# Performance work log

Measured on AMD Instinct MI355X. Metric: run time of the kernel, lower is better.

## Reference

```python
import jax, jax.numpy as jnp
import numpy as np


def _gru_cell(x, h, W_ih, W_hh, b_ih, b_hh):
    # torch.nn.GRUCell math; gate order (r, z, n). x: [.,D] or [1,D] (broadcast), h: [E,D]
    gi = x @ W_ih.T + b_ih            # [., 3D]
    gh = h @ W_hh.T + b_hh            # [E, 3D]
    i_r, i_z, i_n = jnp.split(gi, 3, axis=-1)
    h_r, h_z, h_n = jnp.split(gh, 3, axis=-1)
    r = jax.nn.sigmoid(i_r + h_r)
    z = jax.nn.sigmoid(i_z + h_z)
    n = jnp.tanh(i_n + r * h_n)
    return (1.0 - z) * n + z * h


def setup_inputs() -> dict:
    D = 256          # num_embed_units
    E = 200000       # neighbor edges of the seed
    N = E + 1        # nodes in the sampled subgraph (seed is node E)
    V = 500000       # entity vocab
    R = 1000         # relation vocab
    key = jax.random.key(0)
    ks = jax.random.split(key, 14)
    s = 1.0 / np.sqrt(D)  # torch default init bound
    inp = {
        "encoder_output": jax.random.normal(ks[0], (1, D), jnp.float32),
        "sample_mask": jax.random.normal(ks[1], (1, D), jnp.float32),
        "entity_table": jax.random.normal(ks[2], (V, D), jnp.float32) * 0.02,
        "rel_table": jax.random.normal(ks[3], (R, D), jnp.float32) * 0.02,
        "W_ih": jax.random.uniform(ks[4], (3 * D, D), jnp.float32, -s, s),
        "W_hh": jax.random.uniform(ks[5], (3 * D, D), jnp.float32, -s, s),
        "b_ih": jax.random.uniform(ks[6], (3 * D,), jnp.float32, -s, s),
        "b_hh": jax.random.uniform(ks[7], (3 * D,), jnp.float32, -s, s),
        "sub_W": jax.random.uniform(ks[8], (D, D), jnp.float32, -s, s),
        "sub_b": jax.random.uniform(ks[9], (D,), jnp.float32, -s, s),
        "obj_W": jax.random.uniform(ks[10], (D, D), jnp.float32, -s, s),
        "obj_b": jax.random.uniform(ks[11], (D,), jnp.float32, -s, s),
        "rel_ids": jax.random.randint(ks[12], (E,), 0, R, jnp.int64 if jax.config.jax_enable_x64 else jnp.int32),
        "tail_ids": jnp.arange(E, dtype=jnp.int32),
        "tails_state": jax.random.randint(ks[13], (E,), 0, 2, jnp.int32),
        "origin_ids": jax.random.randint(jax.random.fold_in(key, 99), (E,), 0, V, jnp.int32),
        "seed": E,
        "num_nodes": N,
    }
    return inp


def reference(encoder_output, sample_mask, entity_table, rel_table, W_ih, W_hh, b_ih, b_hh,
              sub_W, sub_b, obj_W, obj_b, rel_ids, tail_ids, tails_state, origin_ids, seed, num_nodes):
    D = encoder_output.shape[-1]
    # seed_state == 0 branch: sub = tanh(Linear(sample_mask))
    sub = jnp.tanh(sample_mask @ sub_W.T + sub_b)                      # [1, D]
    r0 = _gru_cell(encoder_output, sub, W_ih, W_hh, b_ih, b_hh)        # [1, D]
    # vectorized per-edge GRUCell: input r0 (broadcast), hidden = relation embedding
    rel_emb = rel_table[rel_ids]                                       # [E, D]
    rj = _gru_cell(r0, rel_emb, W_ih, W_hh, b_ih, b_hh)                # [E, D]
    obj = jnp.tanh(rj @ obj_W.T + obj_b)                               # [E, D]
    # tails with state==1 get their pretrained entity embedding instead
    from_table = entity_table[origin_ids]                              # [E, D]
    tail_vals = jnp.where((tails_state == 1)[:, None], from_table, obj)
    ent = jnp.zeros((num_nodes, D), dtype=encoder_output.dtype)
    ent = ent.at[seed].set(sub[0])
    ent = ent.at[tail_ids].set(tail_vals)
    return ent
```

## Files before the change

### kernel.cpp

```cpp
#include <hip/hip_runtime.h>
#include <hip/hip_bf16.h>

typedef unsigned short u16;
using bf16x8 = __attribute__((ext_vector_type(8))) short;
using f32x4  = __attribute__((ext_vector_type(4))) float;
using f4     = __attribute__((ext_vector_type(4))) float;

__device__ __forceinline__ u16 f2b(float f) {
    unsigned u = __float_as_uint(f);
    return (u16)((u + 0x7fffu + ((u >> 16) & 1u)) >> 16);
}
__device__ __forceinline__ float sigm(float x) { return 1.f / (1.f + expf(-x)); }

__device__ __forceinline__ bf16x8 pack8(const float* p) {
    float4 a = *(const float4*)p, b = *(const float4*)(p + 4);
    bf16x8 r;
    r[0] = (short)f2b(a.x); r[1] = (short)f2b(a.y);
    r[2] = (short)f2b(a.z); r[3] = (short)f2b(a.w);
    r[4] = (short)f2b(b.x); r[5] = (short)f2b(b.y);
    r[6] = (short)f2b(b.z); r[7] = (short)f2b(b.w);
    return r;
}

__device__ __forceinline__ float dot64(const float* __restrict__ w, const float* s) {
    float acc = 0.f;
    #pragma unroll
    for (int i = 0; i < 16; ++i) {
        float4 v = ((const float4*)w)[i];
        acc += v.x * s[i*4] + v.y * s[i*4+1] + v.z * s[i*4+2] + v.w * s[i*4+3];
    }
    return acc;
}

__global__ __launch_bounds__(256)
void k1a_sub_gi0(const float* __restrict__ enc, const float* __restrict__ mask,
                 const float* __restrict__ W_ih, const float* __restrict__ b_ih,
                 const float* __restrict__ sub_W, const float* __restrict__ sub_b,
                 float* __restrict__ sub_ws, float* __restrict__ gi0,
                 float* __restrict__ out, const int* __restrict__ seed_p)
{
    __shared__ float x_s[256];
    __shared__ float pA[256];
    const int b = blockIdx.x;
    const bool is_sub = (b < 4);
    const int tid = threadIdx.x;
    x_s[tid] = is_sub ? mask[tid] : enc[tid];
    __syncthreads();
    const int t = tid >> 2, g = tid & 3;
    if (is_sub) {
        const int i = b * 64 + t;
        pA[tid] = dot64(sub_W + (size_t)i * 256 + g * 64, x_s + g * 64);
    } else {
        const int j = (b - 4) * 64 + t;
        pA[tid] = dot64(W_ih + (size_t)j * 256 + g * 64, x_s + g * 64);
    }
    __syncthreads();
    if (tid < 64) {
        float v = pA[4*tid] + pA[4*tid+1] + pA[4*tid+2] + pA[4*tid+3];
        if (is_sub) {
            const int i = b * 64 + tid;
            float s = tanhf(v + sub_b[i]);
            sub_ws[i] = s;
            out[(size_t)seed_p[0] * 256 + i] = s;
        } else {
            const int j = (b - 4) * 64 + tid;
            gi0[j] = v + b_ih[j];
        }
    }
}

__global__ __launch_bounds__(256)
void k1b_gh0(const float* __restrict__ sub_ws, const float* __restrict__ W_hh,
             const float* __restrict__ b_hh, float* __restrict__ gh0)
{
    __shared__ float x_s[256];
    __shared__ float pA[256];
    const int tid = threadIdx.x;
    x_s[tid] = sub_ws[tid];
    __syncthreads();
    const int t = tid >> 2, g = tid & 3;
    const int j = blockIdx.x * 64 + t;
    pA[tid] = dot64(W_hh + (size_t)j * 256 + g * 64, x_s + g * 64);
    __syncthreads();
    if (tid < 64) {
        const int jj = blockIdx.x * 64 + tid;
        gh0[jj] = pA[4*tid] + pA[4*tid+1] + pA[4*tid+2] + pA[4*tid+3] + b_hh[jj];
    }
}

__global__ __launch_bounds__(256)
void k1c_gi1(const float* __restrict__ sub_ws, const float* __restrict__ gi0,
             const float* __restrict__ gh0, const float* __restrict__ W_ih,
             const float* __restrict__ b_ih, float* __restrict__ gi1)
{
    __shared__ float r0_s[256];
    __shared__ float pA[256];
    const int tid = threadIdx.x;
    {
        float rr = sigm(gi0[tid]       + gh0[tid]);
        float zz = sigm(gi0[256 + tid] + gh0[256 + tid]);
        float nn = tanhf(gi0[512 + tid] + rr * gh0[512 + tid]);
        r0_s[tid] = (1.f - zz) * nn + zz * sub_ws[tid];
    }
    __syncthreads();
    const int t = tid >> 2, g = tid & 3;
    const int j = blockIdx.x * 64 + t;
    pA[tid] = dot64(W_ih + (size_t)j * 256 + g * 64, r0_s + g * 64);
    __syncthreads();
    if (tid < 64) {
        const int jj = blockIdx.x * 64 + tid;
        gi1[jj] = pA[4*tid] + pA[4*tid+1] + pA[4*tid+2] + pA[4*tid+3] + b_ih[jj];
    }
}

__global__ __launch_bounds__(64)
void k2_ghcomb(const float* __restrict__ rel_table, const float* __restrict__ W_hh,
               const float* __restrict__ b_hh, const float* __restrict__ gi1,
               u16* __restrict__ rj, int R)
{
    const int l = threadIdx.x, m = l & 15, q = l >> 4;
    const int tt = blockIdx.y, jt = blockIdx.x;
    int trow = tt * 16 + m; if (trow >= R) trow = R - 1;
    const int col = jt * 16 + m;
    const float* ab = rel_table + (size_t)trow * 256 + q * 8;
    const float* b0 = W_hh + (size_t)(col      ) * 256 + q * 8;
    const float* b1 = W_hh + (size_t)(col + 256) * 256 + q * 8;
    const float* b2 = W_hh + (size_t)(col + 512) * 256 + q * 8;
    f32x4 aR = {0.f,0.f,0.f,0.f}, aZ = {0.f,0.f,0.f,0.f}, aN = {0.f,0.f,0.f,0.f};
    #pragma unroll
    for (int kk = 0; kk < 8; ++kk) {
        bf16x8 a = pack8(ab + kk * 32);
        aR = __builtin_amdgcn_mfma_f32_16x16x32_bf16(a, pack8(b0 + kk * 32), aR, 0, 0, 0);
        aZ = __builtin_amdgcn_mfma_f32_16x16x32_bf16(a, pack8(b1 + kk * 32), aZ, 0, 0, 0);
        aN = __builtin_amdgcn_mfma_f32_16x16x32_bf16(a, pack8(b2 + kk * 32), aN, 0, 0, 0);
    }
    const float gr = gi1[col], gz = gi1[256 + col], gn = gi1[512 + col];
    const float br = b_hh[col], bz = b_hh[256 + col], bn = b_hh[512 + col];
    #pragma unroll
    for (int i = 0; i < 4; ++i) {
        const int row = tt * 16 + q * 4 + i;
        if (row < R) {
            const float h = rel_table[(size_t)row * 256 + col];
            const float r = sigm(gr + aR[i] + br);
            const float z = sigm(gz + aZ[i] + bz);
            const float n = tanhf(gn + r * (aN[i] + bn));
            rj[(size_t)row * 256 + col] = f2b((1.f - z) * n + z * h);
        }
    }
}

__global__ __launch_bounds__(64)
void k2_obj(const u16* __restrict__ rj, const float* __restrict__ obj_W,
            const float* __restrict__ obj_b, float* __restrict__ obj, int R)
{
    const int l = threadIdx.x, m = l & 15, q = l >> 4;
    const int tt = blockIdx.y, jt = blockIdx.x;
    int trow = tt * 16 + m; if (trow >= R) trow = R - 1;
    const u16* ab = rj + (size_t)trow * 256 + q * 8;
    const float* bb = obj_W + (size_t)(jt * 16 + m) * 256 + q * 8;
    f32x4 acc = {0.f, 0.f, 0.f, 0.f};
    #pragma unroll
    for (int kk = 0; kk < 8; ++kk) {
        bf16x8 a = *(const bf16x8*)(ab + kk * 32);
        bf16x8 b = pack8(bb + kk * 32);
        acc = __builtin_amdgcn_mfma_f32_16x16x32_bf16(a, b, acc, 0, 0, 0);
    }
    const int col = jt * 16 + m;
    const float bias = obj_b[col];
    #pragma unroll
    for (int i = 0; i < 4; ++i) {
        const int row = tt * 16 + q * 4 + i;
        if (row < R) obj[(size_t)row * 256 + col] = tanhf(acc[i] + bias);
    }
}

__global__ __launch_bounds__(256)
void k3_scatter(const float* __restrict__ entity, const float* __restrict__ obj,
                const int* __restrict__ rel_ids, const int* __restrict__ tail_ids,
                const int* __restrict__ state, const int* __restrict__ origin,
                float* __restrict__ out, int E)
{
    const long long gidx = (long long)blockIdx.x * 256 + threadIdx.x;
    const int e = (int)(gidx >> 6);
    if (e >= E) return;
    const int c = ((int)gidx & 63) * 4;
    const float* src = (state[e] == 1) ? entity + (size_t)origin[e] * 256
                                       : obj + (size_t)rel_ids[e] * 256;
    f4 v = *(const f4*)(src + c);
    __builtin_nontemporal_store(v, (f4*)(out + (size_t)tail_ids[e] * 256 + c));
}

extern "C" void kernel_launch(void* const* d_in, const int* in_sizes, int n_in,
                              void* d_out, int out_size, void* d_ws, size_t ws_size,
                              hipStream_t stream)
{
    const float* enc       = (const float*)d_in[0];
    const float* mask      = (const float*)d_in[1];
    const float* entity    = (const float*)d_in[2];
    const float* rel_table = (const float*)d_in[3];
    const float* W_ih      = (const float*)d_in[4];
    const float* W_hh      = (const float*)d_in[5];
    const float* b_ih      = (const float*)d_in[6];
    const float* b_hh      = (const float*)d_in[7];
    const float* sub_W     = (const float*)d_in[8];
    const float* sub_b     = (const float*)d_in[9];
    const float* obj_W     = (const float*)d_in[10];
    const float* obj_b     = (const float*)d_in[11];
    const int* rel_ids     = (const int*)d_in[12];
    const int* tail_ids    = (const int*)d_in[13];
    const int* state       = (const int*)d_in[14];
    const int* origin      = (const int*)d_in[15];
    const int* seed_p      = (const int*)d_in[16];
    float* out = (float*)d_out;

    const int E = in_sizes[12];
    const int R = in_sizes[3] / 256;

    float* ws     = (float*)d_ws;
    float* sub_ws = ws;
    float* gi0    = ws + 256;
    float* gh0    = ws + 1024;
    float* gi1    = ws + 1792;
    u16*   rj     = (u16*)(ws + 2560);
    float* obj    = (float*)((char*)rj + (size_t)R * 256 * 2);

    k1a_sub_gi0<<<16, 256, 0, stream>>>(enc, mask, W_ih, b_ih, sub_W, sub_b,
                                        sub_ws, gi0, out, seed_p);
    k1b_gh0<<<12, 256, 0, stream>>>(sub_ws, W_hh, b_hh, gh0);
    k1c_gi1<<<12, 256, 0, stream>>>(sub_ws, gi0, gh0, W_ih, b_ih, gi1);

    dim3 g_ghc(16, (R + 15) / 16);
    k2_ghcomb<<<g_ghc, 64, 0, stream>>>(rel_table, W_hh, b_hh, gi1, rj, R);
    dim3 g_obj(16, (R + 15) / 16);
    k2_obj<<<g_obj, 64, 0, stream>>>(rj, obj_W, obj_b, obj, R);

    const int blocks = (int)(((long long)E * 64 + 255) / 256);
    k3_scatter<<<blocks, 256, 0, stream>>>(entity, obj, rel_ids, tail_ids,
                                           state, origin, out, E);
}
```

Measured before the change: 713.8 us.

## Fuse GRU gate and obj GEMM kernels, merge head kernels, nontemporal entity loads

Merges the gh0 computation into the first head kernel by having extra blocks recompute sub locally, which removes one launch. Fuses the per-relation GRU combine and the obj projection into one kernel that keeps the bf16 rj tile in shared memory instead of writing it to global memory. The scatter kernel now uses nontemporal loads for entity-table rows. Total time is dominated by the large scatter (about 200 MB of traffic), so the savings are small fixed costs, and the fused kernel launches only about 63 blocks for R=1000.

```diff
diff --git a/kernel.cpp b/kernel.cpp
--- a/kernel.cpp
+++ b/kernel.cpp
@@ -33,63 +33,64 @@
 }
 
 __global__ __launch_bounds__(256)
-void k1a_sub_gi0(const float* __restrict__ enc, const float* __restrict__ mask,
-                 const float* __restrict__ W_ih, const float* __restrict__ b_ih,
-                 const float* __restrict__ sub_W, const float* __restrict__ sub_b,
-                 float* __restrict__ sub_ws, float* __restrict__ gi0,
-                 float* __restrict__ out, const int* __restrict__ seed_p)
-{
-    __shared__ float x_s[256];
-    __shared__ float pA[256];
-    const int b = blockIdx.x;
-    const bool is_sub = (b < 4);
-    const int tid = threadIdx.x;
-    x_s[tid] = is_sub ? mask[tid] : enc[tid];
-    __syncthreads();
+void k_head1(const float* __restrict__ enc, const float* __restrict__ mask,
+             const float* __restrict__ W_ih, const float* __restrict__ b_ih,
+             const float* __restrict__ sub_W, const float* __restrict__ sub_b,
+             const float* __restrict__ W_hh, const float* __restrict__ b_hh,
+             float* __restrict__ sub_ws, float* __restrict__ gi0,
+             float* __restrict__ gh0, float* __restrict__ out,
+             const int* __restrict__ seed_p)
+{
+    __shared__ float x_s[256], pA[256], sub_l[256];
+    const int b = blockIdx.x, tid = threadIdx.x;
     const int t = tid >> 2, g = tid & 3;
-    if (is_sub) {
-        const int i = b * 64 + t;
-        pA[tid] = dot64(sub_W + (size_t)i * 256 + g * 64, x_s + g * 64);
-    } else {
+    if (b < 4) {
+        x_s[tid] = mask[tid];
+        __syncthreads();
+        pA[tid] = dot64(sub_W + (size_t)(b * 64 + t) * 256 + g * 64, x_s + g * 64);
+        __syncthreads();
+        if (tid < 64) {
+            const int i = b * 64 + tid;
+            float s = tanhf(pA[4*tid] + pA[4*tid+1] + pA[4*tid+2] + pA[4*tid+3] + sub_b[i]);
+            sub_ws[i] = s;
+            out[(size_t)seed_p[0] * 256 + i] = s;
+        }
+    } else if (b < 16) {
+        x_s[tid] = enc[tid];
+        __syncthreads();
         const int j = (b - 4) * 64 + t;
         pA[tid] = dot64(W_ih + (size_t)j * 256 + g * 64, x_s + g * 64);
-    }
-    __syncthreads();
-    if (tid < 64) {
-        float v = pA[4*tid] + pA[4*tid+1] + pA[4*tid+2] + pA[4*tid+3];
-        if (is_sub) {
-            const int i = b * 64 + tid;
-            float s = tanhf(v + sub_b[i]);
-            sub_ws[i] = s;
-            out[(size_t)seed_p[0] * 256 + i] = s;
-        } else {
-            const int j = (b - 4) * 64 + tid;
-            gi0[j] = v + b_ih[j];
-        }
-    }
-}
-
-__global__ __launch_bounds__(256)
-void k1b_gh0(const float* __restrict__ sub_ws, const float* __restrict__ W_hh,
-             const float* __restrict__ b_hh, float* __restrict__ gh0)
-{
-    __shared__ float x_s[256];
-    __shared__ float pA[256];
-    const int tid = threadIdx.x;
-    x_s[tid] = sub_ws[tid];
-    __syncthreads();
-    const int t = tid >> 2, g = tid & 3;
-    const int j = blockIdx.x * 64 + t;
-    pA[tid] = dot64(W_hh + (size_t)j * 256 + g * 64, x_s + g * 64);
-    __syncthreads();
-    if (tid < 64) {
-        const int jj = blockIdx.x * 64 + tid;
-        gh0[jj] = pA[4*tid] + pA[4*tid+1] + pA[4*tid+2] + pA[4*tid+3] + b_hh[jj];
-    }
-}
-
-__global__ __launch_bounds__(256)
-void k1c_gi1(const float* __restrict__ sub_ws, const float* __restrict__ gi0,
+        __syncthreads();
+        if (tid < 64) {
+            const int jj = (b - 4) * 64 + tid;
+            gi0[jj] = pA[4*tid] + pA[4*tid+1] + pA[4*tid+2] + pA[4*tid+3] + b_ih[jj];
+        }
+    } else {
+        x_s[tid] = mask[tid];
+        __syncthreads();
+        {
+            float acc = 0.f;
+            const float4* w = (const float4*)(sub_W + (size_t)tid * 256);
+            #pragma unroll
+            for (int i = 0; i < 64; ++i) {
+                float4 v = w[i];
+                acc += v.x * x_s[i*4] + v.y * x_s[i*4+1] + v.z * x_s[i*4+2] + v.w * x_s[i*4+3];
+            }
+            sub_l[tid] = tanhf(acc + sub_b[tid]);
+        }
+        __syncthreads();
+        const int j = (b - 16) * 64 + t;
+        pA[tid] = dot64(W_hh + (size_t)j * 256 + g * 64, sub_l + g * 64);
+        __syncthreads();
+        if (tid < 64) {
+            const int jj = (b - 16) * 64 + tid;
+            gh0[jj] = pA[4*tid] + pA[4*tid+1] + pA[4*tid+2] + pA[4*tid+3] + b_hh[jj];
+        }
+    }
+}
+
+__global__ __launch_bounds__(256)
+void k_head2(const float* __restrict__ sub_ws, const float* __restrict__ gi0,
              const float* __restrict__ gh0, const float* __restrict__ W_ih,
              const float* __restrict__ b_ih, float* __restrict__ gi1)
 {
@@ -113,64 +114,69 @@
     }
 }
 
-__global__ __launch_bounds__(64)
-void k2_ghcomb(const float* __restrict__ rel_table, const float* __restrict__ W_hh,
-               const float* __restrict__ b_hh, const float* __restrict__ gi1,
-               u16* __restrict__ rj, int R)
-{
-    const int l = threadIdx.x, m = l & 15, q = l >> 4;
-    const int tt = blockIdx.y, jt = blockIdx.x;
+__global__ __launch_bounds__(256)
+void k2_fused(const float* __restrict__ rel_table, const float* __restrict__ W_hh,
+              const float* __restrict__ b_hh, const float* __restrict__ gi1,
+              const float* __restrict__ obj_W, const float* __restrict__ obj_b,
+              float* __restrict__ obj, int R)
+{
+    __shared__ u16 rj_s[16][264];
+    const int tid = threadIdx.x;
+    const int wv = tid >> 6, l = tid & 63;
+    const int m = l & 15, q = l >> 4;
+    const int tt = blockIdx.x;
     int trow = tt * 16 + m; if (trow >= R) trow = R - 1;
-    const int col = jt * 16 + m;
     const float* ab = rel_table + (size_t)trow * 256 + q * 8;
-    const float* b0 = W_hh + (size_t)(col      ) * 256 + q * 8;
-    const float* b1 = W_hh + (size_t)(col + 256) * 256 + q * 8;
-    const float* b2 = W_hh + (size_t)(col + 512) * 256 + q * 8;
-    f32x4 aR = {0.f,0.f,0.f,0.f}, aZ = {0.f,0.f,0.f,0.f}, aN = {0.f,0.f,0.f,0.f};
-    #pragma unroll
-    for (int kk = 0; kk < 8; ++kk) {
-        bf16x8 a = pack8(ab + kk * 32);
-        aR = __builtin_amdgcn_mfma_f32_16x16x32_bf16(a, pack8(b0 + kk * 32), aR, 0, 0, 0);
-        aZ = __builtin_amdgcn_mfma_f32_16x16x32_bf16(a, pack8(b1 + kk * 32), aZ, 0, 0, 0);
-        aN = __builtin_amdgcn_mfma_f32_16x16x32_bf16(a, pack8(b2 + kk * 32), aN, 0, 0, 0);
-    }
-    const float gr = gi1[col], gz = gi1[256 + col], gn = gi1[512 + col];
-    const float br = b_hh[col], bz = b_hh[256 + col], bn = b_hh[512 + col];
-    #pragma unroll
-    for (int i = 0; i < 4; ++i) {
-        const int row = tt * 16 + q * 4 + i;
-        if (row < R) {
-            const float h = rel_table[(size_t)row * 256 + col];
+    bf16x8 afr[8];
+    #pragma unroll
+    for (int kk = 0; kk < 8; ++kk) afr[kk] = pack8(ab + kk * 32);
+
+    #pragma unroll
+    for (int jt0 = 0; jt0 < 4; ++jt0) {
+        const int jt  = wv * 4 + jt0;
+        const int col = jt * 16 + m;
+        const float* b0 = W_hh + (size_t)(col      ) * 256 + q * 8;
+        const float* b1 = W_hh + (size_t)(col + 256) * 256 + q * 8;
+        const float* b2 = W_hh + (size_t)(col + 512) * 256 + q * 8;
+        f32x4 aR = {0.f,0.f,0.f,0.f}, aZ = {0.f,0.f,0.f,0.f}, aN = {0.f,0.f,0.f,0.f};
+        #pragma unroll
+        for (int kk = 0; kk < 8; ++kk) {
+            aR = __builtin_amdgcn_mfma_f32_16x16x32_bf16(afr[kk], pack8(b0 + kk * 32), aR, 0, 0, 0);
+            aZ = __builtin_amdgcn_mfma_f32_16x16x32_bf16(afr[kk], pack8(b1 + kk * 32), aZ, 0, 0, 0);
+            aN = __builtin_amdgcn_mfma_f32_16x16x32_bf16(afr[kk], pack8(b2 + kk * 32), aN, 0, 0, 0);
+        }
+        const float gr = gi1[col], gz = gi1[256 + col], gn = gi1[512 + col];
+        const float br = b_hh[col], bz = b_hh[256 + col], bn = b_hh[512 + col];
+        #pragma unroll
+        for (int i = 0; i < 4; ++i) {
+            const int row  = tt * 16 + q * 4 + i;
+            const int hrow = (row < R) ? row : (R - 1);
+            const float h = rel_table[(size_t)hrow * 256 + col];
             const float r = sigm(gr + aR[i] + br);
             const float z = sigm(gz + aZ[i] + bz);
             const float n = tanhf(gn + r * (aN[i] + bn));
-            rj[(size_t)row * 256 + col] = f2b((1.f - z) * n + z * h);
-        }
-    }
-}
-
-__global__ __launch_bounds__(64)
-void k2_obj(const u16* __restrict__ rj, const float* __restrict__ obj_W,
-            const float* __restrict__ obj_b, float* __restrict__ obj, int R)
-{
-    const int l = threadIdx.x, m = l & 15, q = l >> 4;
-    const int tt = blockIdx.y, jt = blockIdx.x;
-    int trow = tt * 16 + m; if (trow >= R) trow = R - 1;
-    const u16* ab = rj + (size_t)trow * 256 + q * 8;
-    const float* bb = obj_W + (size_t)(jt * 16 + m) * 256 + q * 8;
-    f32x4 acc = {0.f, 0.f, 0.f, 0.f};
-    #pragma unroll
-    for (int kk = 0; kk < 8; ++kk) {
-        bf16x8 a = *(const bf16x8*)(ab + kk * 32);
-        bf16x8 b = pack8(bb + kk * 32);
-        acc = __builtin_amdgcn_mfma_f32_16x16x32_bf16(a, b, acc, 0, 0, 0);
-    }
-    const int col = jt * 16 + m;
-    const float bias = obj_b[col];
-    #pragma unroll
-    for (int i = 0; i < 4; ++i) {
-        const int row = tt * 16 + q * 4 + i;
-        if (row < R) obj[(size_t)row * 256 + col] = tanhf(acc[i] + bias);
+            rj_s[q * 4 + i][col] = f2b((1.f - z) * n + z * h);
+        }
+    }
+    __syncthreads();
+
+    #pragma unroll
+    for (int jt0 = 0; jt0 < 4; ++jt0) {
+        const int jt2  = wv * 4 + jt0;
+        const int col2 = jt2 * 16 + m;
+        const float* bb = obj_W + (size_t)col2 * 256 + q * 8;
+        f32x4 acc = {0.f,0.f,0.f,0.f};
+        #pragma unroll
+        for (int kk = 0; kk < 8; ++kk) {
+            bf16x8 a = *(const bf16x8*)&rj_s[m][kk * 32 + q * 8];
+            acc = __builtin_amdgcn_mfma_f32_16x16x32_bf16(a, pack8(bb + kk * 32), acc, 0, 0, 0);
+        }
+        const float bias = obj_b[col2];
+        #pragma unroll
+        for (int i = 0; i < 4; ++i) {
+            const int row = tt * 16 + q * 4 + i;
+            if (row < R) obj[(size_t)row * 256 + col2] = tanhf(acc[i] + bias);
+        }
     }
 }
 
@@ -184,9 +190,12 @@
     const int e = (int)(gidx >> 6);
     if (e >= E) return;
     const int c = ((int)gidx & 63) * 4;
-    const float* src = (state[e] == 1) ? entity + (size_t)origin[e] * 256
-                                       : obj + (size_t)rel_ids[e] * 256;
-    f4 v = *(const f4*)(src + c);
+    f4 v;
+    if (state[e] == 1) {
+        v = __builtin_nontemporal_load((const f4*)(entity + (size_t)origin[e] * 256 + c));
+    } else {
+        v = *(const f4*)(obj + (size_t)rel_ids[e] * 256 + c);
+    }
     __builtin_nontemporal_store(v, (f4*)(out + (size_t)tail_ids[e] * 256 + c));
 }
 
@@ -221,18 +230,14 @@
     float* gi0    = ws + 256;
     float* gh0    = ws + 1024;
     float* gi1    = ws + 1792;
-    u16*   rj     = (u16*)(ws + 2560);
-    float* obj    = (float*)((char*)rj + (size_t)R * 256 * 2);
-
-    k1a_sub_gi0<<<16, 256, 0, stream>>>(enc, mask, W_ih, b_ih, sub_W, sub_b,
-                                        sub_ws, gi0, out, seed_p);
-    k1b_gh0<<<12, 256, 0, stream>>>(sub_ws, W_hh, b_hh, gh0);
-    k1c_gi1<<<12, 256, 0, stream>>>(sub_ws, gi0, gh0, W_ih, b_ih, gi1);
-
-    dim3 g_ghc(16, (R + 15) / 16);
-    k2_ghcomb<<<g_ghc, 64, 0, stream>>>(rel_table, W_hh, b_hh, gi1, rj, R);
-    dim3 g_obj(16, (R + 15) / 16);
-    k2_obj<<<g_obj, 64, 0, stream>>>(rj, obj_W, obj_b, obj, R);
+    float* obj    = ws + 2560;
+
+    k_head1<<<28, 256, 0, stream>>>(enc, mask, W_ih, b_ih, sub_W, sub_b,
+                                    W_hh, b_hh, sub_ws, gi0, gh0, out, seed_p);
+    k_head2<<<12, 256, 0, stream>>>(sub_ws, gi0, gh0, W_ih, b_ih, gi1);
+
+    k2_fused<<<(R + 15) / 16, 256, 0, stream>>>(rel_table, W_hh, b_hh, gi1,
+                                                obj_W, obj_b, obj, R);
 
     const int blocks = (int)(((long long)E * 64 + 255) / 256);
     k3_scatter<<<blocks, 256, 0, stream>>>(entity, obj, rel_ids, tail_ids,
```

After: 752.5 us. 5.4% more time.
